# Kernel tuning notes

Hardware: AMD Instinct MI355X
Metric: run time of the kernel (lower is better)

## Reference

```python
import jax, jax.numpy as jnp
import numpy as np

K = 3
STRIDE = 1


def ste_round(v):
    # Round with straight-through gradient (torch Round Function)
    return v + jax.lax.stop_gradient(jnp.round(v) - v)


def ste_sign(v):
    # Sign with straight-through gradient (torch Sign Function)
    return v + jax.lax.stop_gradient(jnp.sign(v) - v)


def _unfold(x, k, s):
    # torch nn.functional.unfold: [B,C,H,W] -> [B, C*k*k, L], channel-major (c, kh, kw)
    B, C, H, W = x.shape
    Ho = (H - k) // s + 1
    Wo = (W - k) // s + 1
    cols = jnp.stack(
        [x[:, :, i:i + s * Ho:s, j:j + s * Wo:s] for i in range(k) for j in range(k)],
        axis=2,
    )  # [B, C, k*k, Ho, Wo]
    return cols.reshape(B, C * k * k, Ho * Wo)


def reference(x, weight, conv_bias, in_min, in_max, prob_table, rand_idx):
    B = x.shape[0]
    O = weight.shape[0]
    cols = _unfold(x, K, STRIDE)                       # [B, CKK, L]
    CKK = cols.shape[1]
    X = cols.transpose(0, 2, 1).reshape(-1, CKK)       # [N, CKK], N = B*L

    w = ste_sign(weight.reshape(O, CKK))               # ternary weights {-1,0,1}
    wp = jax.nn.relu(w)
    wm = jax.nn.relu(-w)

    scale = in_max - in_min
    Xq = jnp.clip(ste_round((X - in_min) / scale * 15.0), 0.0, 15.0)

    nch = -(-CKK // 4)                                 # ceil(CKK/4)
    pad = nch * 4 - CKK
    if pad:
        Xq = jnp.pad(Xq, ((0, 0), (0, pad)))
        wp = jnp.pad(wp, ((0, 0), (0, pad)))
        wm = jnp.pad(wm, ((0, 0), (0, pad)))

    Xc = Xq.reshape(-1, nch, 4)                        # [N, nch, 4]
    Wp = wp.reshape(O, nch, 4)
    Wm = wm.reshape(O, nch, 4)

    yp = jnp.einsum('nck,ock->cno', Xc, Wp)            # [nch, N, O]
    ym = -jnp.einsum('nck,ock->cno', Xc, Wm)
    T = jnp.stack([yp, ym], axis=1)                    # [nch, 2, N, O]

    longs = jnp.abs(jnp.clip(jnp.round(T), -60.0, 60.0).astype(jnp.int32))
    Q = jnp.clip(ste_round(T / 15.0), -3.0, 3.0)
    temp = prob_table[longs, rand_idx]                 # irregular gather [nch,2,N,O]
    add = temp * jnp.sign(Q) + Q - jax.lax.stop_gradient(Q)

    bias_term = in_min * jnp.sum(w, axis=1)            # linear(InMin*ones, w) -> [O]
    xo = jnp.sum(add, axis=(0, 1)) * scale + bias_term + conv_bias  # [N, O]

    L = X.shape[0] // B
    dim = int(np.sqrt(L))
    return xo.reshape(B, L, O).transpose(0, 2, 1).reshape(B, O, dim, dim)


def setup_inputs() -> dict:
    key = jax.random.key(0)
    k1, k2, k3, k4, k5 = jax.random.split(key, 5)
    B, C, H, W = 2, 16, 66, 66
    O = 64
    CKK = C * K * K            # 144
    nch = -(-CKK // 4)         # 36
    L = ((H - K) // STRIDE + 1) ** 2  # 4096
    N = B * L                  # 8192
    return {
        'x': jax.random.uniform(k1, (B, C, H, W), dtype=jnp.float32),
        'weight': jax.random.normal(k2, (O, C, K, K), dtype=jnp.float32),
        'conv_bias': jax.random.normal(k3, (O,), dtype=jnp.float32),
        'in_min': jnp.zeros((), dtype=jnp.float32),
        'in_max': jnp.ones((), dtype=jnp.float32),
        'prob_table': jax.random.uniform(k4, (61, 1000), dtype=jnp.float32),
        'rand_idx': jax.random.randint(k5, (nch, 2, N, O), 0, 1000, dtype=jnp.int32),
    }
```

## Files before the change

kernel.cpp:

```cpp
#include <hip/hip_runtime.h>

typedef unsigned int uint;

#define B_     2
#define C_     16
#define H_     66
#define W_     66
#define O_     64
#define CKK    144
#define NCH    36
#define DIM    64
#define L_     4096
#define N_     8192
#define PLANE  524288
#define TSTR   1024
#define TROWS  61
#define TCOLS  1000

typedef _Float16 h4 __attribute__((ext_vector_type(4)));

__device__ __forceinline__ void loadg(int (&buf)[16],
                                      const int* __restrict__ rp0,
                                      const int* __restrict__ rp1, int c0) {
#pragma unroll
    for (int j = 0; j < 4; ++j) {
        int c = c0 + j;
        buf[4 * j + 0] = rp0[(2 * c)     * PLANE];
        buf[4 * j + 1] = rp0[(2 * c + 1) * PLANE];
        buf[4 * j + 2] = rp1[(2 * c)     * PLANE];
        buf[4 * j + 3] = rp1[(2 * c + 1) * PLANE];
    }
}

__device__ __forceinline__ void procg(const int (&buf)[16],
                                      const uint*  __restrict__ xq0,
                                      const uint*  __restrict__ xq1,
                                      const uint2* __restrict__ sw,
                                      const _Float16* __restrict__ tbl,
                                      int c0, int o,
                                      float& sum0, float& sum1) {
#pragma unroll
    for (int j = 0; j < 4; ++j) {
        int c = c0 + j;
        uint xv0 = xq0[c];
        uint xv1 = xq1[c];
        uint2 m  = sw[c * O_ + o];
        uint yp0 = ((xv0 & m.x) * 0x01010101u) >> 24;
        uint ym0 = ((xv0 & m.y) * 0x01010101u) >> 24;
        uint yp1 = ((xv1 & m.x) * 0x01010101u) >> 24;
        uint ym1 = ((xv1 & m.y) * 0x01010101u) >> 24;
        sum0 += (float)tbl[(yp0 << 10) + buf[4 * j + 0]];
        sum0 -= (float)tbl[(ym0 << 10) + buf[4 * j + 1]];
        sum1 += (float)tbl[(yp1 << 10) + buf[4 * j + 2]];
        sum1 -= (float)tbl[(ym1 << 10) + buf[4 * j + 3]];
    }
}

__launch_bounds__(1024)
__global__ void k_fused(const float* __restrict__ x,
                        const float* __restrict__ wgt,
                        const float* __restrict__ cbias,
                        const float* __restrict__ pmin,
                        const float* __restrict__ pmax,
                        const float* __restrict__ ptbl,
                        const int*   __restrict__ ridx,
                        float* __restrict__ out) {
    __shared__ __align__(16) _Float16 tbl[TROWS * TSTR];
    __shared__ uint2 s_w[NCH * O_];
    __shared__ float s_bias[O_];
    __shared__ uint  s_xq[2][16 * NCH];

    const int tid = threadIdx.x;
    const float mn = pmin[0];
    const float sc = pmax[0] - mn;

    const int o  = tid & 63;
    const int nl = tid >> 6;
    const int n0 = blockIdx.x * 16 + nl;
    const int n1 = n0 + 4096;
    const int* rp0 = ridx + n0 * O_ + o;
    const int* rp1 = ridx + n1 * O_ + o;
    int A[16], Bb[16];
    loadg(A,  rp0, rp1, 0);
    loadg(Bb, rp0, rp1, 4);

    {
        uint4 z; z.x = z.y = z.z = z.w = 0u;
        uint4* zp = (uint4*)tbl;
        for (int q = tid; q < (TROWS * TSTR) / 8; q += 1024) zp[q] = z;
    }
    __syncthreads();
    for (int q = tid; q < 53 * 250; q += 1024) {
        int r = q / 250, k = q - r * 250;
        float4 v = *(const float4*)(ptbl + (8 + r) * TCOLS + k * 4);
        h4 hh = { (_Float16)v.x, (_Float16)v.y, (_Float16)v.z, (_Float16)v.w };
        *(h4*)(tbl + (8 + r) * TSTR + k * 4) = hh;
    }
    for (int q = tid; q < NCH * O_; q += 1024) {
        int c = q >> 6, oo = q & 63;
        float4 v = *(const float4*)(wgt + oo * CKK + c * 4);
        uint pm = 0, nm = 0;
        if (v.x > 0.0f) pm |= 0x000000FFu; else if (v.x < 0.0f) nm |= 0x000000FFu;
        if (v.y > 0.0f) pm |= 0x0000FF00u; else if (v.y < 0.0f) nm |= 0x0000FF00u;
        if (v.z > 0.0f) pm |= 0x00FF0000u; else if (v.z < 0.0f) nm |= 0x00FF0000u;
        if (v.w > 0.0f) pm |= 0xFF000000u; else if (v.w < 0.0f) nm |= 0xFF000000u;
        s_w[q] = make_uint2(pm, nm);
    }
    for (int i = tid; i < 2 * 16 * NCH; i += 1024) {
        int t  = i / (16 * NCH);
        int r  = i - t * (16 * NCH);
        int nl2 = r / NCH;
        int c2  = r - nl2 * NCH;
        int n2  = blockIdx.x * 16 + nl2 + t * 4096;
        int b2 = n2 >> 12, l2 = n2 & (L_ - 1);
        int h2 = l2 >> 6,  w2 = l2 & (DIM - 1);
        uint packed = 0;
#pragma unroll
        for (int k = 0; k < 4; ++k) {
            int j  = c2 * 4 + k;
            int ci = j / 9;
            int r2 = j - ci * 9;
            int kh = r2 / 3;
            int kw = r2 - kh * 3;
            float v = x[((b2 * C_ + ci) * H_ + (h2 + kh)) * W_ + (w2 + kw)];
            float t2 = (v - mn) / sc * 15.0f;
            float q = fminf(fmaxf(rintf(t2), 0.0f), 15.0f);
            packed |= ((uint)q) << (8 * k);
        }
        s_xq[t][r] = packed;
    }
    if (tid < O_) {
        int sw = 0;
        for (int j = 0; j < CKK; ++j) {
            float v = wgt[tid * CKK + j];
            sw += (v > 0.0f) - (v < 0.0f);
        }
        s_bias[tid] = mn * (float)sw + cbias[tid];
    }
    __syncthreads();

    const uint* xq0 = &s_xq[0][nl * NCH];
    const uint* xq1 = &s_xq[1][nl * NCH];
    const float bo  = s_bias[o];
    float sum0 = 0.0f, sum1 = 0.0f;

    procg(A,  xq0, xq1, s_w, tbl,  0, o, sum0, sum1); loadg(A,  rp0, rp1,  8);
    procg(Bb, xq0, xq1, s_w, tbl,  4, o, sum0, sum1); loadg(Bb, rp0, rp1, 12);
    procg(A,  xq0, xq1, s_w, tbl,  8, o, sum0, sum1); loadg(A,  rp0, rp1, 16);
    procg(Bb, xq0, xq1, s_w, tbl, 12, o, sum0, sum1); loadg(Bb, rp0, rp1, 20);
    procg(A,  xq0, xq1, s_w, tbl, 16, o, sum0, sum1); loadg(A,  rp0, rp1, 24);
    procg(Bb, xq0, xq1, s_w, tbl, 20, o, sum0, sum1); loadg(Bb, rp0, rp1, 28);
    procg(A,  xq0, xq1, s_w, tbl, 24, o, sum0, sum1); loadg(A,  rp0, rp1, 32);
    procg(Bb, xq0, xq1, s_w, tbl, 28, o, sum0, sum1);
    procg(A,  xq0, xq1, s_w, tbl, 32, o, sum0, sum1);

    out[o * L_ + n0]                     = sum0 * sc + bo;
    out[(O_ + o) * L_ + (n1 & (L_ - 1))] = sum1 * sc + bo;
}

extern "C" void kernel_launch(void* const* d_in, const int* in_sizes, int n_in,
                              void* d_out, int out_size, void* d_ws, size_t ws_size,
                              hipStream_t stream) {
    const float* x     = (const float*)d_in[0];
    const float* wgt   = (const float*)d_in[1];
    const float* cbias = (const float*)d_in[2];
    const float* pmin  = (const float*)d_in[3];
    const float* pmax  = (const float*)d_in[4];
    const float* ptbl  = (const float*)d_in[5];
    const int*   ridx  = (const int*)d_in[6];
    float* out = (float*)d_out;

    k_fused<<<256, 1024, 0, stream>>>(x, wgt, cbias, pmin, pmax, ptbl, ridx, out);
}
```

Measured before the change: 38.14 us.

## Quantize prob table to 8-bit and split chunk planes across waves

Stores the probability table as 8-bit values scaled by 255 instead of fp16, so the LDS footprint is smaller, and accumulates in integers. Each block now covers 32 consecutive outputs. Each wave handles 9 of the 72 (chunk, sign) planes for 16 positions, so each thread's random-index loads read 16 positions per plane. Partial sums go through a shared slab and a cross-wave reduction. The 8-bit table adds rounding error to every gathered probability, which may break tolerance. It also needs an extra barrier and reduction pass.

```diff
diff --git a/kernel.cpp b/kernel.cpp
--- a/kernel.cpp
+++ b/kernel.cpp
@@ -1,6 +1,7 @@
 #include <hip/hip_runtime.h>
 
 typedef unsigned int uint;
+typedef unsigned char u8;
 
 #define B_     2
 #define C_     16
@@ -13,48 +14,9 @@
 #define L_     4096
 #define N_     8192
 #define PLANE  524288
+#define NB     32
 #define TSTR   1024
-#define TROWS  61
 #define TCOLS  1000
-
-typedef _Float16 h4 __attribute__((ext_vector_type(4)));
-
-__device__ __forceinline__ void loadg(int (&buf)[16],
-                                      const int* __restrict__ rp0,
-                                      const int* __restrict__ rp1, int c0) {
-#pragma unroll
-    for (int j = 0; j < 4; ++j) {
-        int c = c0 + j;
-        buf[4 * j + 0] = rp0[(2 * c)     * PLANE];
-        buf[4 * j + 1] = rp0[(2 * c + 1) * PLANE];
-        buf[4 * j + 2] = rp1[(2 * c)     * PLANE];
-        buf[4 * j + 3] = rp1[(2 * c + 1) * PLANE];
-    }
-}
-
-__device__ __forceinline__ void procg(const int (&buf)[16],
-                                      const uint*  __restrict__ xq0,
-                                      const uint*  __restrict__ xq1,
-                                      const uint2* __restrict__ sw,
-                                      const _Float16* __restrict__ tbl,
-                                      int c0, int o,
-                                      float& sum0, float& sum1) {
-#pragma unroll
-    for (int j = 0; j < 4; ++j) {
-        int c = c0 + j;
-        uint xv0 = xq0[c];
-        uint xv1 = xq1[c];
-        uint2 m  = sw[c * O_ + o];
-        uint yp0 = ((xv0 & m.x) * 0x01010101u) >> 24;
-        uint ym0 = ((xv0 & m.y) * 0x01010101u) >> 24;
-        uint yp1 = ((xv1 & m.x) * 0x01010101u) >> 24;
-        uint ym1 = ((xv1 & m.y) * 0x01010101u) >> 24;
-        sum0 += (float)tbl[(yp0 << 10) + buf[4 * j + 0]];
-        sum0 -= (float)tbl[(ym0 << 10) + buf[4 * j + 1]];
-        sum1 += (float)tbl[(yp1 << 10) + buf[4 * j + 2]];
-        sum1 -= (float)tbl[(ym1 << 10) + buf[4 * j + 3]];
-    }
-}
 
 __launch_bounds__(1024)
 __global__ void k_fused(const float* __restrict__ x,
@@ -65,36 +27,45 @@
                         const float* __restrict__ ptbl,
                         const int*   __restrict__ ridx,
                         float* __restrict__ out) {
-    __shared__ __align__(16) _Float16 tbl[TROWS * TSTR];
+    __shared__ __align__(16) u8 tbl[54 * TSTR];
     __shared__ uint2 s_w[NCH * O_];
+    __shared__ uint  s_xq[NB * NCH];
+    __shared__ short slab[16][16][66];
     __shared__ float s_bias[O_];
-    __shared__ uint  s_xq[2][16 * NCH];
 
     const int tid = threadIdx.x;
+    const int wv  = tid >> 6;
+    const int o   = tid & 63;
+    const int h16 = (wv & 1) << 4;
+    const int p0  = 9 * (wv >> 1);
+    const int nb0 = blockIdx.x * NB;
+
     const float mn = pmin[0];
     const float sc = pmax[0] - mn;
 
-    const int o  = tid & 63;
-    const int nl = tid >> 6;
-    const int n0 = blockIdx.x * 16 + nl;
-    const int n1 = n0 + 4096;
-    const int* rp0 = ridx + n0 * O_ + o;
-    const int* rp1 = ridx + n1 * O_ + o;
-    int A[16], Bb[16];
-    loadg(A,  rp0, rp1, 0);
-    loadg(Bb, rp0, rp1, 4);
+    const int* rbase = ridx + (nb0 + h16) * O_ + o;
 
-    {
+    int idxA[16], idxB[16];
+#define LOADU(BUF, J)                                                    \
+    {                                                                    \
+        const int* ptr = rbase + (p0 + (J)) * PLANE;                     \
+        _Pragma("unroll")                                                \
+        for (int k = 0; k < 16; ++k) BUF[k] = ptr[k * O_];               \
+    }
+
+    LOADU(idxA, 0)
+    LOADU(idxB, 1)
+
+    if (tid < 64) {
         uint4 z; z.x = z.y = z.z = z.w = 0u;
-        uint4* zp = (uint4*)tbl;
-        for (int q = tid; q < (TROWS * TSTR) / 8; q += 1024) zp[q] = z;
+        ((uint4*)tbl)[tid] = z;
     }
-    __syncthreads();
     for (int q = tid; q < 53 * 250; q += 1024) {
         int r = q / 250, k = q - r * 250;
         float4 v = *(const float4*)(ptbl + (8 + r) * TCOLS + k * 4);
-        h4 hh = { (_Float16)v.x, (_Float16)v.y, (_Float16)v.z, (_Float16)v.w };
-        *(h4*)(tbl + (8 + r) * TSTR + k * 4) = hh;
+        uint b0 = (uint)rintf(v.x * 255.f), b1 = (uint)rintf(v.y * 255.f);
+        uint b2 = (uint)rintf(v.z * 255.f), b3 = (uint)rintf(v.w * 255.f);
+        *(uint*)(tbl + (r + 1) * TSTR + k * 4) = b0 | (b1 << 8) | (b2 << 16) | (b3 << 24);
     }
     for (int q = tid; q < NCH * O_; q += 1024) {
         int c = q >> 6, oo = q & 63;
@@ -106,12 +77,10 @@
         if (v.w > 0.0f) pm |= 0xFF000000u; else if (v.w < 0.0f) nm |= 0xFF000000u;
         s_w[q] = make_uint2(pm, nm);
     }
-    for (int i = tid; i < 2 * 16 * NCH; i += 1024) {
-        int t  = i / (16 * NCH);
-        int r  = i - t * (16 * NCH);
-        int nl2 = r / NCH;
-        int c2  = r - nl2 * NCH;
-        int n2  = blockIdx.x * 16 + nl2 + t * 4096;
+    for (int i = tid; i < NB * NCH; i += 1024) {
+        int nl2 = i / NCH;
+        int c2  = i - nl2 * NCH;
+        int n2  = nb0 + nl2;
         int b2 = n2 >> 12, l2 = n2 & (L_ - 1);
         int h2 = l2 >> 6,  w2 = l2 & (DIM - 1);
         uint packed = 0;
@@ -127,7 +96,7 @@
             float q = fminf(fmaxf(rintf(t2), 0.0f), 15.0f);
             packed |= ((uint)q) << (8 * k);
         }
-        s_xq[t][r] = packed;
+        s_xq[i] = packed;
     }
     if (tid < O_) {
         int sw = 0;
@@ -139,23 +108,55 @@
     }
     __syncthreads();
 
-    const uint* xq0 = &s_xq[0][nl * NCH];
-    const uint* xq1 = &s_xq[1][nl * NCH];
-    const float bo  = s_bias[o];
-    float sum0 = 0.0f, sum1 = 0.0f;
+    const u8* tb = tbl - 7 * TSTR;
+    int acc[16];
+#pragma unroll
+    for (int k = 0; k < 16; ++k) acc[k] = 0;
 
-    procg(A,  xq0, xq1, s_w, tbl,  0, o, sum0, sum1); loadg(A,  rp0, rp1,  8);
-    procg(Bb, xq0, xq1, s_w, tbl,  4, o, sum0, sum1); loadg(Bb, rp0, rp1, 12);
-    procg(A,  xq0, xq1, s_w, tbl,  8, o, sum0, sum1); loadg(A,  rp0, rp1, 16);
-    procg(Bb, xq0, xq1, s_w, tbl, 12, o, sum0, sum1); loadg(Bb, rp0, rp1, 20);
-    procg(A,  xq0, xq1, s_w, tbl, 16, o, sum0, sum1); loadg(A,  rp0, rp1, 24);
-    procg(Bb, xq0, xq1, s_w, tbl, 20, o, sum0, sum1); loadg(Bb, rp0, rp1, 28);
-    procg(A,  xq0, xq1, s_w, tbl, 24, o, sum0, sum1); loadg(A,  rp0, rp1, 32);
-    procg(Bb, xq0, xq1, s_w, tbl, 28, o, sum0, sum1);
-    procg(A,  xq0, xq1, s_w, tbl, 32, o, sum0, sum1);
+#define PROCU(BUF, J)                                                    \
+    {                                                                    \
+        const int p = p0 + (J);                                          \
+        const uint2 mm = s_w[(p >> 1) * O_ + o];                         \
+        const uint m = (p & 1) ? mm.y : mm.x;                            \
+        const int sm = (p & 1) ? -1 : 0;                                 \
+        _Pragma("unroll")                                                \
+        for (int k = 0; k < 16; ++k) {                                   \
+            uint xv = s_xq[(h16 + k) * NCH + (p >> 1)];                  \
+            uint y = ((xv & m) * 0x01010101u) >> 24;                     \
+            uint row = y < 7u ? 7u : y;                                  \
+            int v = (int)tb[(row << 10) + (uint)BUF[k]];                 \
+            acc[k] += (v ^ sm) - sm;                                     \
+        }                                                                \
+    }
 
-    out[o * L_ + n0]                     = sum0 * sc + bo;
-    out[(O_ + o) * L_ + (n1 & (L_ - 1))] = sum1 * sc + bo;
+    PROCU(idxA, 0) LOADU(idxA, 2)
+    PROCU(idxB, 1) LOADU(idxB, 3)
+    PROCU(idxA, 2) LOADU(idxA, 4)
+    PROCU(idxB, 3) LOADU(idxB, 5)
+    PROCU(idxA, 4) LOADU(idxA, 6)
+    PROCU(idxB, 5) LOADU(idxB, 7)
+    PROCU(idxA, 6) LOADU(idxA, 8)
+    PROCU(idxB, 7)
+    PROCU(idxA, 8)
+
+#pragma unroll
+    for (int k = 0; k < 16; ++k) slab[wv][k][o] = (short)acc[k];
+    __syncthreads();
+
+    const int ro = tid >> 4;
+    const int rn = tid & 15;
+    int s0 = 0, s1 = 0;
+#pragma unroll
+    for (int w2 = 0; w2 < 8; ++w2) {
+        s0 += slab[2 * w2][rn][ro];
+        s1 += slab[2 * w2 + 1][rn][ro];
+    }
+    const float k255 = sc * (1.0f / 255.0f);
+    const float bo   = s_bias[ro];
+    const int   b    = nb0 >> 12;
+    const int   lb   = nb0 & (L_ - 1);
+    out[(b * O_ + ro) * L_ + lb + rn]      = (float)s0 * k255 + bo;
+    out[(b * O_ + ro) * L_ + lb + rn + 16] = (float)s1 * k255 + bo;
 }
 
 extern "C" void kernel_launch(void* const* d_in, const int* in_sizes, int n_in,
```

Result: no change. 38.36 us (+0.6%).
